# Kernel tuning notes

Hardware: AMD Instinct MI355X
Metric: run time of the kernel (lower is better)

The kernel has to match this reference:

```python
import jax, jax.numpy as jnp
import numpy as np

# Llama-3-8B-like attention, prefill over B sequences of length S (flattened tokens)
D = 4096      # hidden_size
N = 32        # num query heads
K = 8         # num KV heads (GQA)
H = 128       # head_dim (== head_dim_original, already a multiple of 128 so no padding)
B = 4         # sequences in the ragged batch
S = 1024      # tokens per sequence
T = B * S     # total flattened tokens
ROPE_THETA = 10000.0


def _apply_rope(x, positions, head_dim, theta):
    # x: [T, n_heads, H]; positions: [T] int
    inv_freq = 1.0 / (theta ** (jnp.arange(0, head_dim, 2, dtype=jnp.float32) / head_dim))
    freqs = positions.astype(jnp.float32)[:, None] * inv_freq[None, :]  # [T, H/2]
    emb = jnp.concatenate([freqs, freqs], axis=-1)                       # [T, H]
    cos = jnp.cos(emb)[:, None, :].astype(x.dtype)
    sin = jnp.sin(emb)[:, None, :].astype(x.dtype)
    x1, x2 = jnp.split(x, 2, axis=-1)
    rotated = jnp.concatenate([-x2, x1], axis=-1)
    return x * cos + rotated * sin


def setup_inputs() -> dict:
    key = jax.random.key(0)
    ks = jax.random.split(key, 5)
    x = jax.random.normal(ks[0], (T, D), dtype=jnp.float32)
    # positions restart per sequence (ragged prefill metadata)
    input_positions = (jnp.arange(T, dtype=jnp.int32) % S)
    w_scale = 0.02
    Wq = jax.random.normal(ks[1], (D, N, H), dtype=jnp.float32) * w_scale
    Wk = jax.random.normal(ks[2], (D, K, H), dtype=jnp.float32) * w_scale
    Wv = jax.random.normal(ks[3], (D, K, H), dtype=jnp.float32) * w_scale
    Wo = jax.random.normal(ks[4], (N, H, D), dtype=jnp.float32) * w_scale
    return {"x": x, "input_positions": input_positions,
            "Wq": Wq, "Wk": Wk, "Wv": Wv, "Wo": Wo}


def reference(x, input_positions, Wq, Wk, Wv, Wo):
    # QKV projections (flattened tokens)
    q = jnp.einsum('td,dnh->tnh', x, Wq)   # [T, N, H]
    k = jnp.einsum('td,dkh->tkh', x, Wk)   # [T, K, H]
    v = jnp.einsum('td,dkh->tkh', x, Wv)   # [T, K, H]
    q = _apply_rope(q, input_positions, H, ROPE_THETA)
    k = _apply_rope(k, input_positions, H, ROPE_THETA)

    # Ragged causal attention: per-sequence causal SDPA with GQA head grouping.
    G = N // K  # query heads per KV head
    qb = q.reshape(B, S, K, G, H)
    kb = k.reshape(B, S, K, H)
    vb = v.reshape(B, S, K, H)
    scale = jnp.asarray(H, q.dtype) ** -0.5  # head_dim_original ** -0.5
    scores = jnp.einsum('bqkgh,bskh->bkgqs', qb, kb) * scale  # [B,K,G,S,S]
    causal = jnp.tril(jnp.ones((S, S), dtype=bool))
    scores = jnp.where(causal, scores, jnp.finfo(scores.dtype).min)
    probs = jax.nn.softmax(scores, axis=-1)
    out = jnp.einsum('bkgqs,bskh->bqkgh', probs, vb).reshape(T, N, H)

    # Output projection
    o = jnp.einsum('tnh,nhd->td', out, Wo)  # [T, D]
    return o
```

## Files before the change

### kernel.cpp

```cpp
#include <hip/hip_runtime.h>
#include <cstdint>


typedef unsigned short u16;
typedef short bf16x8 __attribute__((ext_vector_type(8)));
typedef float f32x4 __attribute__((ext_vector_type(4)));

#define L2E 1.44269504088896340736f

static __device__ __forceinline__ u16 f2bf(float f) {
  union { float f; unsigned u; } v; v.f = f;
  unsigned r = (v.u + 0x7fffu + ((v.u >> 16) & 1u)) >> 16;
  return (u16)r;
}
static __device__ __forceinline__ float bf2f(u16 h) {
  union { unsigned u; float f; } v; v.u = ((unsigned)h) << 16;
  return v.f;
}

typedef __attribute__((address_space(1))) const unsigned int gas_u32;
typedef __attribute__((address_space(3))) unsigned int las_u32;
static __device__ __forceinline__ void glds16(const void* g, const void* l) {
  __builtin_amdgcn_global_load_lds((gas_u32*)(uintptr_t)g,
                                   (las_u32*)(unsigned)(uintptr_t)l, 16, 0, 0);
}

__global__ __launch_bounds__(256) void cvt_kernel(const float4* __restrict__ in,
                                                  uint2* __restrict__ out, int n4) {
  int i = blockIdx.x * 256 + threadIdx.x;
  if (i < n4) {
    float4 v = in[i];
    uint2 r;
    r.x = (unsigned)f2bf(v.x) | ((unsigned)f2bf(v.y) << 16);
    r.y = (unsigned)f2bf(v.z) | ((unsigned)f2bf(v.w) << 16);
    out[i] = r;
  }
}

__global__ __launch_bounds__(256) void tcvt_kernel(const float* __restrict__ in,
                                                   u16* __restrict__ out, int R, int C) {
  __shared__ float tile[32][33];
  int tx = threadIdx.x, ty = threadIdx.y;
  int r0 = blockIdx.y * 32, c0 = blockIdx.x * 32;
#pragma unroll
  for (int j = 0; j < 4; ++j)
    tile[ty + j * 8][tx] = in[(size_t)(r0 + ty + j * 8) * C + c0 + tx];
  __syncthreads();
#pragma unroll
  for (int j = 0; j < 4; ++j)
    out[(size_t)(c0 + ty + j * 8) * R + r0 + tx] = f2bf(tile[tx][ty + j * 8]);
}

template <int BF16OUT>
__global__ __launch_bounds__(256, 2) void gemm_nt(const u16* __restrict__ A,
                                                  const u16* __restrict__ Bm,
                                                  void* __restrict__ Cp,
                                                  int M, int N, int Kd) {
  __shared__ u16 Al[128 * 64];
  __shared__ u16 Bl[128 * 64];
  const int tid = threadIdx.x;
  const int w = tid >> 6, lane = tid & 63;
  const int ln15 = lane & 15, quad = lane >> 4;
  const int wm = w & 1, wn = w >> 1;
  const int m0 = blockIdx.y * 128, n0 = blockIdx.x * 128;

  const int rA = w * 8 + (lane >> 3);
  const int cA = (((lane & 7) ^ (rA & 7)) << 3);
  const u16* aptr = A + (size_t)(m0 + rA) * Kd + cA;
  const u16* bptr = Bm + (size_t)(n0 + rA) * Kd + cA;

  f32x4 acc[4][4];
#pragma unroll
  for (int i = 0; i < 4; ++i)
#pragma unroll
    for (int j = 0; j < 4; ++j) acc[i][j] = f32x4{0.f, 0.f, 0.f, 0.f};

  for (int k0 = 0; k0 < Kd; k0 += 64) {
    __syncthreads();
#pragma unroll
    for (int q = 0; q < 4; ++q) {
      glds16(aptr + (size_t)q * 32 * Kd, &Al[(q * 32 + w * 8) * 64]);
      glds16(bptr + (size_t)q * 32 * Kd, &Bl[(q * 32 + w * 8) * 64]);
    }
    aptr += 64; bptr += 64;
    __syncthreads();
#pragma unroll
    for (int ks = 0; ks < 2; ++ks) {
      bf16x8 af[4], bfr[4];
#pragma unroll
      for (int t = 0; t < 4; ++t) {
        int ra = wm * 64 + t * 16 + ln15;
        int pa = (ks * 4 + quad) ^ (ra & 7);
        af[t] = *(const bf16x8*)&Al[ra * 64 + pa * 8];
        int rb = wn * 64 + t * 16 + ln15;
        int pb = (ks * 4 + quad) ^ (rb & 7);
        bfr[t] = *(const bf16x8*)&Bl[rb * 64 + pb * 8];
      }
#pragma unroll
      for (int mt = 0; mt < 4; ++mt)
#pragma unroll
        for (int nt = 0; nt < 4; ++nt)
          acc[mt][nt] =
              __builtin_amdgcn_mfma_f32_16x16x32_bf16(af[mt], bfr[nt], acc[mt][nt], 0, 0, 0);
    }
  }

#pragma unroll
  for (int mt = 0; mt < 4; ++mt) {
#pragma unroll
    for (int nt = 0; nt < 4; ++nt) {
      int row = m0 + wm * 64 + mt * 16 + quad * 4;
      int col = n0 + wn * 64 + nt * 16 + ln15;
#pragma unroll
      for (int r = 0; r < 4; ++r) {
        float v = acc[mt][nt][r];
        if (BF16OUT)
          ((u16*)Cp)[(size_t)(row + r) * N + col] = f2bf(v);
        else
          ((float*)Cp)[(size_t)(row + r) * N + col] = v;
      }
    }
  }
}

__global__ __launch_bounds__(256) void rope_kernel(u16* __restrict__ qkv,
                                                   const int* __restrict__ pos, int total) {
  int idx = blockIdx.x * 256 + threadIdx.x;
  if (idx >= total) return;
  int t = idx / 2560;
  int rem = idx - t * 2560;
  int head = rem >> 6;
  int i = rem & 63;
  float p = (float)pos[t];
  float inv = exp2f(-0.20751874963942190927f * (float)i);
  float f = p * inv;
  float s, c;
  sincosf(f, &s, &c);
  int colbase = (head < 32) ? head * 128 : (4096 + (head - 32) * 128);
  u16* base = qkv + (size_t)t * 6144 + colbase;
  float x1 = bf2f(base[i]), x2 = bf2f(base[i + 64]);
  float o1 = x1 * c - x2 * s;
  float o2 = x2 * c + x1 * s;
  if (head < 32) { o1 *= 0.08838834764831845f; o2 *= 0.08838834764831845f; }
  base[i] = f2bf(o1);
  base[i + 64] = f2bf(o2);
}

__global__ __launch_bounds__(256, 3) void attn_kernel(const u16* __restrict__ qkv,
                                                      u16* __restrict__ outp) {
  __shared__ u16 Klds[64 * 128];
  __shared__ u16 Vtlds[128 * 72];
  __shared__ u16 Plds[4 * 16 * 72];

  const int bx = blockIdx.x;
  const int qb = 15 - (bx & 15);
  const int n = (bx >> 4) & 31;
  const int b = bx >> 9;
  const int kh = n >> 2;

  const int tid = threadIdx.x;
  const int w = tid >> 6;
  const int lane = tid & 63;
  const int ln15 = lane & 15;
  const int quad = lane >> 4;

  const int ldq = 6144;
  const int seq0 = b << 10;
  const int q0 = seq0 + qb * 64;

  const u16* Qg = qkv + n * 128;
  const u16* Kg = qkv + 4096 + kh * 128;
  const u16* Vg = qkv + 5120 + kh * 128;

  bf16x8 qf[4];
  {
    const u16* qrow = Qg + (size_t)(q0 + w * 16 + ln15) * ldq + quad * 8;
#pragma unroll
    for (int ks = 0; ks < 4; ++ks) qf[ks] = *(const bf16x8*)(qrow + ks * 32);
  }

  f32x4 o[8];
#pragma unroll
  for (int i = 0; i < 8; ++i) o[i] = f32x4{0.f, 0.f, 0.f, 0.f};
  float m_r[4] = {-INFINITY, -INFINITY, -INFINITY, -INFINITY};
  float l_r[4] = {0.f, 0.f, 0.f, 0.f};

  const int krow = w * 4 + (lane >> 4);
  const int kcol = (((lane & 15) ^ (krow & 7)) << 3);

  const int vs0 = (lane & 31) * 2;
  const int vhb = w * 32 + (lane >> 5) * 16;

  for (int kt = 0; kt <= qb; ++kt) {
    __syncthreads();
    {
      const u16* kbase = Kg + (size_t)(seq0 + kt * 64 + krow) * ldq + kcol;
#pragma unroll
      for (int q = 0; q < 4; ++q)
        glds16(kbase + (size_t)q * 16 * ldq, &Klds[(q * 16 + w * 4) * 128]);
    }
    {
      const u16* v0 = Vg + (size_t)(seq0 + kt * 64 + vs0) * ldq + vhb;
      union { uint4 v[2]; u16 s[16]; } ra, rb;
      ra.v[0] = *(const uint4*)v0;
      ra.v[1] = *(const uint4*)(v0 + 8);
      rb.v[0] = *(const uint4*)(v0 + ldq);
      rb.v[1] = *(const uint4*)(v0 + ldq + 8);
#pragma unroll
      for (int j = 0; j < 16; ++j) {
        unsigned pk = (unsigned)ra.s[j] | ((unsigned)rb.s[j] << 16);
        *(unsigned*)&Vtlds[(vhb + j) * 72 + vs0] = pk;
      }
    }
    __syncthreads();

    f32x4 sfr[4];
#pragma unroll
    for (int c = 0; c < 4; ++c) {
      f32x4 acc = f32x4{0.f, 0.f, 0.f, 0.f};
#pragma unroll
      for (int ks = 0; ks < 4; ++ks) {
        int rr = c * 16 + ln15;
        int ph = (ks * 4 + quad) ^ (rr & 7);
        bf16x8 kf = *(const bf16x8*)&Klds[rr * 128 + ph * 8];
        acc = __builtin_amdgcn_mfma_f32_16x16x32_bf16(qf[ks], kf, acc, 0, 0, 0);
      }
      sfr[c] = acc;
    }

    if (kt == qb) {
#pragma unroll
      for (int c = 0; c < 4; ++c) {
        int col = c * 16 + ln15;
#pragma unroll
        for (int r = 0; r < 4; ++r)
          if (col > w * 16 + quad * 4 + r) sfr[c][r] = -INFINITY;
      }
    }

    float alpha[4];
#pragma unroll
    for (int r = 0; r < 4; ++r) {
      float mx = fmaxf(fmaxf(sfr[0][r], sfr[1][r]), fmaxf(sfr[2][r], sfr[3][r]));
      mx = fmaxf(mx, __shfl_xor(mx, 1));
      mx = fmaxf(mx, __shfl_xor(mx, 2));
      mx = fmaxf(mx, __shfl_xor(mx, 4));
      mx = fmaxf(mx, __shfl_xor(mx, 8));
      float mnew = fmaxf(m_r[r], mx);
      alpha[r] = exp2f((m_r[r] - mnew) * L2E);
      m_r[r] = mnew;
      float rs = 0.f;
#pragma unroll
      for (int c = 0; c < 4; ++c) {
        float pv = exp2f((sfr[c][r] - mnew) * L2E);
        sfr[c][r] = pv;
        rs += pv;
      }
      rs += __shfl_xor(rs, 1);
      rs += __shfl_xor(rs, 2);
      rs += __shfl_xor(rs, 4);
      rs += __shfl_xor(rs, 8);
      l_r[r] = alpha[r] * l_r[r] + rs;
    }

#pragma unroll
    for (int ht = 0; ht < 8; ++ht)
#pragma unroll
      for (int r = 0; r < 4; ++r) o[ht][r] *= alpha[r];

#pragma unroll
    for (int c = 0; c < 4; ++c)
#pragma unroll
      for (int r = 0; r < 4; ++r)
        Plds[w * 1152 + (quad * 4 + r) * 72 + c * 16 + ln15] = f2bf(sfr[c][r]);

    asm volatile("s_waitcnt lgkmcnt(0)" ::: "memory");

    bf16x8 pf[2];
#pragma unroll
    for (int ks = 0; ks < 2; ++ks)
      pf[ks] = *(const bf16x8*)&Plds[w * 1152 + ln15 * 72 + ks * 32 + quad * 8];
#pragma unroll
    for (int ht = 0; ht < 8; ++ht) {
#pragma unroll
      for (int ks = 0; ks < 2; ++ks) {
        bf16x8 vf = *(const bf16x8*)&Vtlds[(ht * 16 + ln15) * 72 + ks * 32 + quad * 8];
        o[ht] = __builtin_amdgcn_mfma_f32_16x16x32_bf16(pf[ks], vf, o[ht], 0, 0, 0);
      }
    }
  }

#pragma unroll
  for (int r = 0; r < 4; ++r) l_r[r] = 1.f / l_r[r];
#pragma unroll
  for (int ht = 0; ht < 8; ++ht)
#pragma unroll
    for (int r = 0; r < 4; ++r)
      outp[(size_t)(q0 + w * 16 + quad * 4 + r) * 4096 + n * 128 + ht * 16 + ln15] =
          f2bf(o[ht][r] * l_r[r]);
}

extern "C" void kernel_launch(void* const* d_in, const int* in_sizes, int n_in,
                              void* d_out, int out_size, void* d_ws, size_t ws_size,
                              hipStream_t stream) {
  const float* x = (const float*)d_in[0];
  const int* posi = (const int*)d_in[1];
  const float* Wq = (const float*)d_in[2];
  const float* Wk = (const float*)d_in[3];
  const float* Wv = (const float*)d_in[4];
  const float* Wo = (const float*)d_in[5];
  float* out = (float*)d_out;
  char* ws = (char*)d_ws;

  u16* xb = (u16*)(ws);
  u16* Wt = (u16*)(ws + 33554432);
  u16* WoT = (u16*)(ws + 83886080);
  u16* qkv = (u16*)(ws + 117440512);
  u16* attn = xb;

  cvt_kernel<<<16384, 256, 0, stream>>>((const float4*)x, (uint2*)xb, 4194304);
  tcvt_kernel<<<dim3(128, 128), dim3(32, 8), 0, stream>>>(Wq, Wt, 4096, 4096);
  tcvt_kernel<<<dim3(32, 128), dim3(32, 8), 0, stream>>>(Wk, Wt + (size_t)4096 * 4096, 4096, 1024);
  tcvt_kernel<<<dim3(32, 128), dim3(32, 8), 0, stream>>>(Wv, Wt + (size_t)5120 * 4096, 4096, 1024);
  tcvt_kernel<<<dim3(128, 128), dim3(32, 8), 0, stream>>>(Wo, WoT, 4096, 4096);

  gemm_nt<1><<<dim3(48, 32), 256, 0, stream>>>(xb, Wt, qkv, 4096, 6144, 4096);
  rope_kernel<<<40960, 256, 0, stream>>>(qkv, posi, 10485760);
  attn_kernel<<<2048, 256, 0, stream>>>(qkv, attn);
  gemm_nt<0><<<dim3(32, 32), 256, 0, stream>>>(attn, WoT, out, 4096, 4096, 4096);
}
```

Before: 768.0 us.

## Double attention query tile per block and loop RoPE over heads per thread

```diff
diff --git a/kernel.cpp b/kernel.cpp
--- a/kernel.cpp
+++ b/kernel.cpp
@@ -124,38 +124,39 @@
 }
 
 __global__ __launch_bounds__(256) void rope_kernel(u16* __restrict__ qkv,
-                                                   const int* __restrict__ pos, int total) {
+                                                   const int* __restrict__ pos) {
   int idx = blockIdx.x * 256 + threadIdx.x;
-  if (idx >= total) return;
-  int t = idx / 2560;
-  int rem = idx - t * 2560;
-  int head = rem >> 6;
-  int i = rem & 63;
+  int t = idx >> 6;
+  int i = idx & 63;
   float p = (float)pos[t];
   float inv = exp2f(-0.20751874963942190927f * (float)i);
-  float f = p * inv;
   float s, c;
-  sincosf(f, &s, &c);
-  int colbase = (head < 32) ? head * 128 : (4096 + (head - 32) * 128);
-  u16* base = qkv + (size_t)t * 6144 + colbase;
-  float x1 = bf2f(base[i]), x2 = bf2f(base[i + 64]);
-  float o1 = x1 * c - x2 * s;
-  float o2 = x2 * c + x1 * s;
-  if (head < 32) { o1 *= 0.08838834764831845f; o2 *= 0.08838834764831845f; }
-  base[i] = f2bf(o1);
-  base[i + 64] = f2bf(o2);
+  sincosf(p * inv, &s, &c);
+  u16* base = qkv + (size_t)t * 6144 + i;
+  const float qs = 0.08838834764831845f;
+#pragma unroll 8
+  for (int head = 0; head < 40; ++head) {
+    int colbase = (head < 32) ? head * 128 : (4096 + (head - 32) * 128);
+    u16* bp = base + colbase;
+    float x1 = bf2f(bp[0]), x2 = bf2f(bp[64]);
+    float o1 = x1 * c - x2 * s;
+    float o2 = x2 * c + x1 * s;
+    if (head < 32) { o1 *= qs; o2 *= qs; }
+    bp[0] = f2bf(o1);
+    bp[64] = f2bf(o2);
+  }
 }
 
 __global__ __launch_bounds__(256, 3) void attn_kernel(const u16* __restrict__ qkv,
                                                       u16* __restrict__ outp) {
   __shared__ u16 Klds[64 * 128];
   __shared__ u16 Vtlds[128 * 72];
-  __shared__ u16 Plds[4 * 16 * 72];
+  __shared__ u16 Plds[4 * 32 * 72];
 
   const int bx = blockIdx.x;
-  const int qb = 15 - (bx & 15);
-  const int n = (bx >> 4) & 31;
-  const int b = bx >> 9;
+  const int qb = 7 - (bx & 7);
+  const int n = (bx >> 3) & 31;
+  const int b = bx >> 8;
   const int kh = n >> 2;
 
   const int tid = threadIdx.x;
@@ -166,24 +167,31 @@
 
   const int ldq = 6144;
   const int seq0 = b << 10;
-  const int q0 = seq0 + qb * 64;
+  const int ql0 = qb * 128 + w * 32;
+  const int q0g = seq0 + qb * 128;
 
   const u16* Qg = qkv + n * 128;
   const u16* Kg = qkv + 4096 + kh * 128;
   const u16* Vg = qkv + 5120 + kh * 128;
 
-  bf16x8 qf[4];
-  {
-    const u16* qrow = Qg + (size_t)(q0 + w * 16 + ln15) * ldq + quad * 8;
-#pragma unroll
-    for (int ks = 0; ks < 4; ++ks) qf[ks] = *(const bf16x8*)(qrow + ks * 32);
-  }
-
-  f32x4 o[8];
-#pragma unroll
-  for (int i = 0; i < 8; ++i) o[i] = f32x4{0.f, 0.f, 0.f, 0.f};
-  float m_r[4] = {-INFINITY, -INFINITY, -INFINITY, -INFINITY};
-  float l_r[4] = {0.f, 0.f, 0.f, 0.f};
+  bf16x8 qf[2][4];
+#pragma unroll
+  for (int mt = 0; mt < 2; ++mt) {
+    const u16* qrow = Qg + (size_t)(q0g + w * 32 + mt * 16 + ln15) * ldq + quad * 8;
+#pragma unroll
+    for (int ks = 0; ks < 4; ++ks) qf[mt][ks] = *(const bf16x8*)(qrow + ks * 32);
+  }
+
+  f32x4 o[2][8];
+#pragma unroll
+  for (int mt = 0; mt < 2; ++mt)
+#pragma unroll
+    for (int i = 0; i < 8; ++i) o[mt][i] = f32x4{0.f, 0.f, 0.f, 0.f};
+  float m_r[2][4], l_r[2][4];
+#pragma unroll
+  for (int mt = 0; mt < 2; ++mt)
+#pragma unroll
+    for (int r = 0; r < 4; ++r) { m_r[mt][r] = -INFINITY; l_r[mt][r] = 0.f; }
 
   const int krow = w * 4 + (lane >> 4);
   const int kcol = (((lane & 15) ^ (krow & 7)) << 3);
@@ -191,7 +199,8 @@
   const int vs0 = (lane & 31) * 2;
   const int vhb = w * 32 + (lane >> 5) * 16;
 
-  for (int kt = 0; kt <= qb; ++kt) {
+  const int ktiles = 2 * qb + 2;
+  for (int kt = 0; kt < ktiles; ++kt) {
     __syncthreads();
     {
       const u16* kbase = Kg + (size_t)(seq0 + kt * 64 + krow) * ldq + kcol;
@@ -214,90 +223,112 @@
     }
     __syncthreads();
 
-    f32x4 sfr[4];
-#pragma unroll
-    for (int c = 0; c < 4; ++c) {
-      f32x4 acc = f32x4{0.f, 0.f, 0.f, 0.f};
-#pragma unroll
-      for (int ks = 0; ks < 4; ++ks) {
-        int rr = c * 16 + ln15;
-        int ph = (ks * 4 + quad) ^ (rr & 7);
-        bf16x8 kf = *(const bf16x8*)&Klds[rr * 128 + ph * 8];
-        acc = __builtin_amdgcn_mfma_f32_16x16x32_bf16(qf[ks], kf, acc, 0, 0, 0);
-      }
-      sfr[c] = acc;
-    }
-
-    if (kt == qb) {
+    if (kt * 64 > ql0 + 31) continue;
+
+    f32x4 sfr[2][4];
+#pragma unroll
+    for (int mt = 0; mt < 2; ++mt)
 #pragma unroll
       for (int c = 0; c < 4; ++c) {
-        int col = c * 16 + ln15;
+        f32x4 acc = f32x4{0.f, 0.f, 0.f, 0.f};
+#pragma unroll
+        for (int ks = 0; ks < 4; ++ks) {
+          int rr = c * 16 + ln15;
+          int ph = (ks * 4 + quad) ^ (rr & 7);
+          bf16x8 kf = *(const bf16x8*)&Klds[rr * 128 + ph * 8];
+          acc = __builtin_amdgcn_mfma_f32_16x16x32_bf16(qf[mt][ks], kf, acc, 0, 0, 0);
+        }
+        sfr[mt][c] = acc;
+      }
+
+#pragma unroll
+    for (int mt = 0; mt < 2; ++mt) {
+      if (kt * 64 + 63 > ql0 + mt * 16) {
+#pragma unroll
+        for (int c = 0; c < 4; ++c) {
+          int col = kt * 64 + c * 16 + ln15;
+#pragma unroll
+          for (int r = 0; r < 4; ++r)
+            if (col > ql0 + mt * 16 + quad * 4 + r) sfr[mt][c][r] = -INFINITY;
+        }
+      }
+    }
+
+    float alpha[2][4];
+#pragma unroll
+    for (int mt = 0; mt < 2; ++mt)
+#pragma unroll
+      for (int r = 0; r < 4; ++r) {
+        float mx = fmaxf(fmaxf(sfr[mt][0][r], sfr[mt][1][r]),
+                         fmaxf(sfr[mt][2][r], sfr[mt][3][r]));
+        mx = fmaxf(mx, __shfl_xor(mx, 1));
+        mx = fmaxf(mx, __shfl_xor(mx, 2));
+        mx = fmaxf(mx, __shfl_xor(mx, 4));
+        mx = fmaxf(mx, __shfl_xor(mx, 8));
+        float mnew = fmaxf(m_r[mt][r], mx);
+        alpha[mt][r] = exp2f((m_r[mt][r] - mnew) * L2E);
+        m_r[mt][r] = mnew;
+        float rs = 0.f;
+#pragma unroll
+        for (int c = 0; c < 4; ++c) {
+          float pv = exp2f((sfr[mt][c][r] - mnew) * L2E);
+          sfr[mt][c][r] = pv;
+          rs += pv;
+        }
+        rs += __shfl_xor(rs, 1);
+        rs += __shfl_xor(rs, 2);
+        rs += __shfl_xor(rs, 4);
+        rs += __shfl_xor(rs, 8);
+        l_r[mt][r] = alpha[mt][r] * l_r[mt][r] + rs;
+      }
+
+#pragma unroll
+    for (int mt = 0; mt < 2; ++mt)
+#pragma unroll
+      for (int ht = 0; ht < 8; ++ht)
+#pragma unroll
+        for (int r = 0; r < 4; ++r) o[mt][ht][r] *= alpha[mt][r];
+
+#pragma unroll
+    for (int mt = 0; mt < 2; ++mt)
+#pragma unroll
+      for (int c = 0; c < 4; ++c)
 #pragma unroll
         for (int r = 0; r < 4; ++r)
-          if (col > w * 16 + quad * 4 + r) sfr[c][r] = -INFINITY;
-      }
-    }
-
-    float alpha[4];
-#pragma unroll
-    for (int r = 0; r < 4; ++r) {
-      float mx = fmaxf(fmaxf(sfr[0][r], sfr[1][r]), fmaxf(sfr[2][r], sfr[3][r]));
-      mx = fmaxf(mx, __shfl_xor(mx, 1));
-      mx = fmaxf(mx, __shfl_xor(mx, 2));
-      mx = fmaxf(mx, __shfl_xor(mx, 4));
-      mx = fmaxf(mx, __shfl_xor(mx, 8));
-      float mnew = fmaxf(m_r[r], mx);
-      alpha[r] = exp2f((m_r[r] - mnew) * L2E);
-      m_r[r] = mnew;
-      float rs = 0.f;
-#pragma unroll
-      for (int c = 0; c < 4; ++c) {
-        float pv = exp2f((sfr[c][r] - mnew) * L2E);
-        sfr[c][r] = pv;
-        rs += pv;
-      }
-      rs += __shfl_xor(rs, 1);
-      rs += __shfl_xor(rs, 2);
-      rs += __shfl_xor(rs, 4);
-      rs += __shfl_xor(rs, 8);
-      l_r[r] = alpha[r] * l_r[r] + rs;
-    }
-
+          Plds[w * 2304 + (mt * 16 + quad * 4 + r) * 72 + c * 16 + ln15] =
+              f2bf(sfr[mt][c][r]);
+
+    asm volatile("s_waitcnt lgkmcnt(0)" ::: "memory");
+
+#pragma unroll
+    for (int mt = 0; mt < 2; ++mt) {
+      bf16x8 pf[2];
+#pragma unroll
+      for (int ks = 0; ks < 2; ++ks)
+        pf[ks] = *(const bf16x8*)&Plds[w * 2304 + (mt * 16 + ln15) * 72 + ks * 32 + quad * 8];
+#pragma unroll
+      for (int ht = 0; ht < 8; ++ht) {
+#pragma unroll
+        for (int ks = 0; ks < 2; ++ks) {
+          bf16x8 vf = *(const bf16x8*)&Vtlds[(ht * 16 + ln15) * 72 + ks * 32 + quad * 8];
+          o[mt][ht] = __builtin_amdgcn_mfma_f32_16x16x32_bf16(pf[ks], vf, o[mt][ht], 0, 0, 0);
+        }
+      }
+    }
+  }
+
+#pragma unroll
+  for (int mt = 0; mt < 2; ++mt)
+#pragma unroll
+    for (int r = 0; r < 4; ++r) l_r[mt][r] = 1.f / l_r[mt][r];
+#pragma unroll
+  for (int mt = 0; mt < 2; ++mt)
 #pragma unroll
     for (int ht = 0; ht < 8; ++ht)
 #pragma unroll
-      for (int r = 0; r < 4; ++r) o[ht][r] *= alpha[r];
-
-#pragma unroll
-    for (int c = 0; c < 4; ++c)
-#pragma unroll
       for (int r = 0; r < 4; ++r)
-        Plds[w * 1152 + (quad * 4 + r) * 72 + c * 16 + ln15] = f2bf(sfr[c][r]);
-
-    asm volatile("s_waitcnt lgkmcnt(0)" ::: "memory");
-
-    bf16x8 pf[2];
-#pragma unroll
-    for (int ks = 0; ks < 2; ++ks)
-      pf[ks] = *(const bf16x8*)&Plds[w * 1152 + ln15 * 72 + ks * 32 + quad * 8];
-#pragma unroll
-    for (int ht = 0; ht < 8; ++ht) {
-#pragma unroll
-      for (int ks = 0; ks < 2; ++ks) {
-        bf16x8 vf = *(const bf16x8*)&Vtlds[(ht * 16 + ln15) * 72 + ks * 32 + quad * 8];
-        o[ht] = __builtin_amdgcn_mfma_f32_16x16x32_bf16(pf[ks], vf, o[ht], 0, 0, 0);
-      }
-    }
-  }
-
-#pragma unroll
-  for (int r = 0; r < 4; ++r) l_r[r] = 1.f / l_r[r];
-#pragma unroll
-  for (int ht = 0; ht < 8; ++ht)
-#pragma unroll
-    for (int r = 0; r < 4; ++r)
-      outp[(size_t)(q0 + w * 16 + quad * 4 + r) * 4096 + n * 128 + ht * 16 + ln15] =
-          f2bf(o[ht][r] * l_r[r]);
+        outp[(size_t)(q0g + w * 32 + mt * 16 + quad * 4 + r) * 4096 + n * 128 + ht * 16 + ln15] =
+            f2bf(o[mt][ht][r] * l_r[mt][r]);
 }
 
 extern "C" void kernel_launch(void* const* d_in, const int* in_sizes, int n_in,
@@ -325,7 +356,7 @@
   tcvt_kernel<<<dim3(128, 128), dim3(32, 8), 0, stream>>>(Wo, WoT, 4096, 4096);
 
   gemm_nt<1><<<dim3(48, 32), 256, 0, stream>>>(xb, Wt, qkv, 4096, 6144, 4096);
-  rope_kernel<<<40960, 256, 0, stream>>>(qkv, posi, 10485760);
-  attn_kernel<<<2048, 256, 0, stream>>>(qkv, attn);
+  rope_kernel<<<1024, 256, 0, stream>>>(qkv, posi);
+  attn_kernel<<<1024, 256, 0, stream>>>(qkv, attn);
   gemm_nt<0><<<dim3(32, 32), 256, 0, stream>>>(attn, WoT, out, 4096, 4096, 4096);
 }
```

Measured after the change: 950.7 us. 23.8% more time.
